# Performance work log

Measured on AMD Instinct MI355X. Metric: run time of the kernel, lower is better.

Reference implementation:

```python
import jax, jax.numpy as jnp
import numpy as np

N = 4096        # nodes
E = 131072      # edges (avg degree 32)
D = 128         # parser.d
H1, H2, H3 = 256, 128, 64   # parser.neurons_gnn
L = 2
THRESH = 0.6 ** L           # cosine-similarity cutoff used in attention()
SCALE = 0.05                # weight init scale


def setup_inputs() -> dict:
    key = jax.random.key(0)
    ks = jax.random.split(key, 14)
    X = jax.random.normal(ks[0], (N, D), dtype=jnp.float32)
    edge_index = jax.random.randint(ks[1], (2, E), 0, N, dtype=jnp.int64)
    W1 = jax.random.normal(ks[2], (D, H1), dtype=jnp.float32) * SCALE
    b1 = jnp.zeros((H1,), dtype=jnp.float32)
    a1w = jax.random.normal(ks[3], (2 * H1,), dtype=jnp.float32) * SCALE
    a1b = jnp.zeros((), dtype=jnp.float32)
    W2 = jax.random.normal(ks[4], (H1, H2), dtype=jnp.float32) * SCALE
    b2 = jnp.zeros((H2,), dtype=jnp.float32)
    a2w = jax.random.normal(ks[5], (2 * H2,), dtype=jnp.float32) * SCALE
    a2b = jnp.zeros((), dtype=jnp.float32)
    W3 = jax.random.normal(ks[6], (H2, H3), dtype=jnp.float32) * SCALE
    b3 = jnp.zeros((H3,), dtype=jnp.float32)
    return {"X": X, "edge_index": edge_index,
            "W1": W1, "b1": b1, "a1w": a1w, "a1b": a1b,
            "W2": W2, "b2": b2, "a2w": a2w, "a2b": a2b,
            "W3": W3, "b3": b3}


def _attention(h, src, dst, aw, ab):
    """Vectorized form of GNN.attention: edge-softmax neighbor aggregation
    plus dense cosine-thresholded all-pairs aggregation, averaged.
    attn_fc(cat(h_i, h_j)) = (h_i . aw_left) + (h_j . aw_right) + ab."""
    n, dh = h.shape
    al = h @ aw[:dh]            # [N] left half of attention projection
    ar = h @ aw[dh:]            # [N] right half
    # --- neighbor branch: a_ij = softmax-like normalized exp(leaky_relu(.)) over neighbors of i
    e = jnp.exp(jax.nn.leaky_relu(al[src] + ar[dst] + ab))   # [E]
    denom = jax.ops.segment_sum(e, src, num_segments=n)      # [N]
    a = e / denom[src]                                       # [E]
    h_a = h + jax.ops.segment_sum(a[:, None] * h[dst], src, num_segments=n)
    # --- dense branch: thresholded cosine similarity modulates attention score
    hn = h / jnp.linalg.norm(h, axis=1, keepdims=True)       # [N, dh]
    C = hn @ hn.T                                            # [N, N] cosine
    C = jnp.where(C <= THRESH, 0.0, C)
    S = al[:, None] + ar[None, :] + ab                       # [N, N] attn scores
    B = jnp.exp(C * jax.nn.leaky_relu(S))                    # [N, N]
    h1 = h + B @ h
    return 0.5 * (h_a + h1)


def reference(X, edge_index, W1, b1, a1w, a1b, W2, b2, a2w, a2b, W3, b3):
    src, dst = edge_index[0], edge_index[1]
    h = X @ W1 + b1
    h = _attention(h, src, dst, a1w, a1b)
    h = jax.nn.relu(h)
    h = h @ W2 + b2
    h = _attention(h, src, dst, a2w, a2b)
    h = jax.nn.relu(h)
    h = h @ W3 + b3
    # F.normalize(h, p=2, dim=1)
    h = h / jnp.maximum(jnp.linalg.norm(h, axis=1, keepdims=True), 1e-12)
    return h
```

## Files before the change

### kernel.cpp

```cpp
#include <hip/hip_runtime.h>
#include <math.h>
#include <type_traits>

#define NN 4096
#define NE 131072

typedef short short8 __attribute__((ext_vector_type(8)));
typedef float f32x4 __attribute__((ext_vector_type(4)));
typedef float f32x2 __attribute__((ext_vector_type(2)));
typedef unsigned short u16;

__device__ __forceinline__ float lrelu_f(float x) { return x > 0.0f ? x : 0.01f * x; }

__device__ __forceinline__ u16 f2bf(float x) {
  unsigned int u = __float_as_uint(x);
  unsigned int r = (u + 0x7FFF + ((u >> 16) & 1)) >> 16;
  return (u16)r;
}
__device__ __forceinline__ float bf2f(u16 b) { return __uint_as_float(((unsigned int)b) << 16); }

__device__ __forceinline__ void gload_lds16(const u16* g, u16* l) {
  __builtin_amdgcn_global_load_lds((const __attribute__((address_space(1))) void*)g,
                                   (__attribute__((address_space(3))) void*)l, 16, 0, 0);
}

__global__ __launch_bounds__(256) void wtrans_all_kernel(
    const float* __restrict__ W1, const float* __restrict__ W2, const float* __restrict__ W3,
    u16* __restrict__ w1h, u16* __restrict__ w1l,
    u16* __restrict__ w2h, u16* __restrict__ w2l,
    u16* __restrict__ w3h, u16* __restrict__ w3l) {
  __shared__ u16 th[32][33], tl[32][33];
  const float* W; u16 *oh, *ol; int K, P, bp, bk;
  int bx = blockIdx.x;
  if (bx < 32)      { W = W1; oh = w1h; ol = w1l; K = 128; P = 256; int b = bx;      bp = b & 7; bk = b >> 3; }
  else if (bx < 64) { W = W2; oh = w2h; ol = w2l; K = 256; P = 128; int b = bx - 32; bp = b & 3; bk = b >> 2; }
  else              { W = W3; oh = w3h; ol = w3l; K = 128; P = 64;  int b = bx - 64; bp = b & 1; bk = b >> 1; }
  int t = threadIdx.x, tx = t & 31, ty8 = t >> 5;
  #pragma unroll
  for (int r = 0; r < 4; ++r) {
    int k = bk * 32 + ty8 + r * 8;
    int p = bp * 32 + tx;
    float x = W[(size_t)k * P + p];
    u16 hi = f2bf(x);
    th[ty8 + r * 8][tx] = hi;
    tl[ty8 + r * 8][tx] = f2bf(x - bf2f(hi));
  }
  __syncthreads();
  #pragma unroll
  for (int r = 0; r < 4; ++r) {
    int p = bp * 32 + ty8 + r * 8;
    int k = bk * 32 + tx;
    oh[(size_t)p * K + k] = th[tx][ty8 + r * 8];
    ol[(size_t)p * K + k] = tl[tx][ty8 + r * 8];
  }
}

template<int K, int P, bool RELU, bool NORM>
__global__ __launch_bounds__(256) void mgemm_kernel(
    const float* __restrict__ A,
    const u16* __restrict__ WThi, const u16* __restrict__ WTlo,
    const float* __restrict__ bias, float* __restrict__ O) {
  constexpr int KC = K / 32;
  __shared__ float ldsn[4][16];
  int w = threadIdx.x >> 6, l = threadIdx.x & 63;
  int lr = l & 15, lk = l >> 4;
  int i0 = blockIdx.x * 16;
  int p0 = blockIdx.y * 64 + w * 16;
  const float* ar_ = A + (size_t)(i0 + lr) * K + lk * 8;
  const u16* brh = WThi + (size_t)(p0 + lr) * K + lk * 8;
  const u16* brl = WTlo + (size_t)(p0 + lr) * K + lk * 8;
  f32x4 ahh = {0.f, 0.f, 0.f, 0.f};
  f32x4 ahl = {0.f, 0.f, 0.f, 0.f};
  f32x4 alh = {0.f, 0.f, 0.f, 0.f};
  #pragma unroll
  for (int c = 0; c < KC; ++c) {
    f32x4 a0 = *(const f32x4*)(ar_ + 32 * c);
    f32x4 a1 = *(const f32x4*)(ar_ + 32 * c + 4);
    float av[8] = {a0[0], a0[1], a0[2], a0[3], a1[0], a1[1], a1[2], a1[3]};
    short8 Ah, Al;
    #pragma unroll
    for (int j = 0; j < 8; ++j) {
      float x = av[j];
      if (RELU) x = fmaxf(x, 0.0f);
      u16 hi = f2bf(x);
      Ah[j] = (short)hi;
      Al[j] = (short)f2bf(x - bf2f(hi));
    }
    short8 Bh = *(const short8*)(brh + 32 * c);
    short8 Bl = *(const short8*)(brl + 32 * c);
    ahh = __builtin_amdgcn_mfma_f32_16x16x32_bf16(Ah, Bh, ahh, 0, 0, 0);
    ahl = __builtin_amdgcn_mfma_f32_16x16x32_bf16(Ah, Bl, ahl, 0, 0, 0);
    alh = __builtin_amdgcn_mfma_f32_16x16x32_bf16(Al, Bh, alh, 0, 0, 0);
  }
  int p = p0 + lr;
  float bv = bias[p];
  float ov[4];
  #pragma unroll
  for (int q = 0; q < 4; ++q) ov[q] = ahh[q] + ahl[q] + alh[q] + bv;

  if (NORM) {
    float sq[4];
    #pragma unroll
    for (int q = 0; q < 4; ++q) {
      float s = ov[q] * ov[q];
      #pragma unroll
      for (int m = 1; m < 16; m <<= 1) s += __shfl_xor(s, m);
      sq[q] = s;
    }
    if (lr == 0) {
      #pragma unroll
      for (int q = 0; q < 4; ++q) ldsn[w][4 * lk + q] = sq[q];
    }
    __syncthreads();
    #pragma unroll
    for (int q = 0; q < 4; ++q) {
      int row = 4 * lk + q;
      float n2 = ldsn[0][row] + ldsn[1][row] + ldsn[2][row] + ldsn[3][row];
      float nf = 1.0f / fmaxf(sqrtf(n2), 1e-12f);
      int i = i0 + row;
      O[(size_t)i * P + p] = ov[q] * nf;
    }
  } else {
    #pragma unroll
    for (int q = 0; q < 4; ++q) {
      int i = i0 + 4 * lk + q;
      O[(size_t)i * P + p] = ov[q];
    }
  }
}

template<int DH>
__global__ __launch_bounds__(256) void prep_kernel(const float* __restrict__ h,
    const float* __restrict__ aw, float* __restrict__ al, float* __restrict__ ar,
    float* __restrict__ inv, float* __restrict__ cs,
    u16* __restrict__ hhi, u16* __restrict__ hlo, u16* __restrict__ hT) {
  constexpr int CPT = DH / 16;
  __shared__ u16 tile[16][DH + 8];
  __shared__ float ldsp[4][DH];
  int t = threadIdx.x;
  int w = t >> 6, l = t & 63;
  int rw = l >> 4;
  int row = w * 4 + rw;
  int tcol = l & 15;
  int i = blockIdx.x * 16 + row;
  int c0 = tcol * CPT;

  float v[CPT];
  const float* hr = h + (size_t)i * DH + c0;
  #pragma unroll
  for (int k = 0; k < CPT; k += 4) {
    f32x4 x = *(const f32x4*)(hr + k);
    v[k] = x[0]; v[k + 1] = x[1]; v[k + 2] = x[2]; v[k + 3] = x[3];
  }
  float s2 = 0.f, sl = 0.f, sr = 0.f;
  #pragma unroll
  for (int k = 0; k < CPT; ++k) {
    s2 = fmaf(v[k], v[k], s2);
    sl = fmaf(v[k], aw[c0 + k], sl);
    sr = fmaf(v[k], aw[DH + c0 + k], sr);
  }
  #pragma unroll
  for (int m = 1; m < 16; m <<= 1) {
    s2 += __shfl_xor(s2, m);
    sl += __shfl_xor(sl, m);
    sr += __shfl_xor(sr, m);
  }
  if (tcol == 0) { al[i] = sl; ar[i] = sr; inv[i] = rsqrtf(s2); }

  short8 hs[CPT / 8], ls[CPT / 8];
  #pragma unroll
  for (int k = 0; k < CPT; ++k) {
    float x = v[k];
    u16 hi = f2bf(x);
    hs[k / 8][k & 7] = (short)hi;
    ls[k / 8][k & 7] = (short)f2bf(x - bf2f(hi));
  }
  #pragma unroll
  for (int b = 0; b < CPT / 8; ++b) {
    *(short8*)&hhi[(size_t)i * DH + c0 + b * 8] = hs[b];
    *(short8*)&hlo[(size_t)i * DH + c0 + b * 8] = ls[b];
    *(short8*)&tile[row][c0 + b * 8] = hs[b];
  }
  float colp[CPT];
  #pragma unroll
  for (int k = 0; k < CPT; ++k) {
    float s = v[k];
    s += __shfl_xor(s, 16);
    s += __shfl_xor(s, 32);
    colp[k] = s;
  }
  if (rw == 0) {
    #pragma unroll
    for (int k = 0; k < CPT; ++k) ldsp[w][c0 + k] = colp[k];
  }
  __syncthreads();
  if (t < DH) {
    float s = ldsp[0][t] + ldsp[1][t] + ldsp[2][t] + ldsp[3][t];
    atomicAdd(&cs[t], s);
    int i0 = blockIdx.x * 16;
    short8 o0, o1;
    #pragma unroll
    for (int r = 0; r < 8; ++r) o0[r] = (short)tile[r][t];
    #pragma unroll
    for (int r = 0; r < 8; ++r) o1[r] = (short)tile[8 + r][t];
    *(short8*)&hT[(size_t)t * NN + i0] = o0;
    *(short8*)&hT[(size_t)t * NN + i0 + 8] = o1;
  }
}

__global__ void hist_kernel(const int* __restrict__ src, int* __restrict__ counts) {
  int e = blockIdx.x * 256 + threadIdx.x;
  atomicAdd(&counts[src[e]], 1);
}

__global__ __launch_bounds__(1024) void scan_kernel(const int* __restrict__ counts,
    int* __restrict__ offsets, int* __restrict__ cursor) {
  __shared__ int part[1024];
  int t = threadIdx.x;
  int v[4]; int run = 0;
  #pragma unroll
  for (int j = 0; j < 4; ++j) { v[j] = counts[4 * t + j]; run += v[j]; }
  part[t] = run;
  __syncthreads();
  for (int off = 1; off < 1024; off <<= 1) {
    int y = (t >= off) ? part[t - off] : 0;
    __syncthreads();
    part[t] += y;
    __syncthreads();
  }
  int base = part[t] - run;
  #pragma unroll
  for (int j = 0; j < 4; ++j) { offsets[4 * t + j] = base; cursor[4 * t + j] = base; base += v[j]; }
  if (t == 1023) offsets[NN] = base;
}

__global__ void scatter_idx_kernel(const int* __restrict__ src, const int* __restrict__ dst,
    int* __restrict__ cursor, int* __restrict__ dstS) {
  int e = blockIdx.x * 256 + threadIdx.x;
  int s = src[e];
  int p = atomicAdd(&cursor[s], 1);
  dstS[p] = dst[e];
}

template<int DH>
__global__ __launch_bounds__(256) void gather_kernel(const float* __restrict__ h,
    const int* __restrict__ offsets, const int* __restrict__ dstS,
    const float* __restrict__ al, const float* __restrict__ ar,
    const float* __restrict__ ab, float* __restrict__ o) {
  constexpr int VW = DH / 64;
  using V = typename std::conditional<VW == 4, f32x4, f32x2>::type;
  int wid = threadIdx.x >> 6, lane = threadIdx.x & 63;
  int i = blockIdx.x * 4 + wid;
  int beg = offsets[i], end = offsets[i + 1];
  float base = al[i] + ab[0];
  V acc0{}, acc1{};
  float esum0 = 0.f, esum1 = 0.f;
  int k = beg;
  for (; k + 2 <= end; k += 2) {
    int d0 = dstS[k], d1 = dstS[k + 1];
    float e0 = expf(lrelu_f(base + ar[d0]));
    float e1 = expf(lrelu_f(base + ar[d1]));
    V v0 = *(const V*)&h[(size_t)d0 * DH + lane * VW];
    V v1 = *(const V*)&h[(size_t)d1 * DH + lane * VW];
    esum0 += e0; esum1 += e1;
    acc0 += e0 * v0;
    acc1 += e1 * v1;
  }
  if (k < end) {
    int d0 = dstS[k];
    float e0 = expf(lrelu_f(base + ar[d0]));
    V v0 = *(const V*)&h[(size_t)d0 * DH + lane * VW];
    esum0 += e0;
    acc0 += e0 * v0;
  }
  float esum = esum0 + esum1;
  float rd = (beg < end) ? 0.5f / esum : 0.0f;
  *(V*)&o[(size_t)i * DH + lane * VW] = (acc0 + acc1) * rd;
}

template<int DH>
__global__ __launch_bounds__(256) void qk_kernel(
    const u16* __restrict__ hhi, const u16* __restrict__ hlo,
    const float* __restrict__ al, const float* __restrict__ ar,
    const float* __restrict__ inv, const float* __restrict__ ab,
    u16* __restrict__ W, int* __restrict__ flags) {
  constexpr int KC = DH / 32;
  __shared__ u16 sA[2][2][128][32];
  __shared__ u16 sB[2][2][128][32];
  int i0 = blockIdx.x * 128;
  int j0 = blockIdx.y * 128;
  int w = threadIdx.x >> 6, l = threadIdx.x & 63;
  int wr = w >> 1, wc = w & 1;
  int lr = l & 15, lk = l >> 4;

  int rl = l >> 2;
  int sc = ((l & 3) ^ ((l >> 3) & 3)) * 8;
  const u16* gAh0 = hhi + (size_t)(i0 + 32 * w + rl) * DH + sc;
  const u16* gAl0 = hlo + (size_t)(i0 + 32 * w + rl) * DH + sc;
  const u16* gBh0 = hhi + (size_t)(j0 + 32 * w + rl) * DH + sc;
  const u16* gBl0 = hlo + (size_t)(j0 + 32 * w + rl) * DH + sc;

  f32x4 acc[4][4];
  #pragma unroll
  for (int q = 0; q < 4; ++q)
    #pragma unroll
    for (int s = 0; s < 4; ++s) acc[q][s] = (f32x4){0.f, 0.f, 0.f, 0.f};

#define QK_STAGE(buf, c) do { \
    gload_lds16(gAh0 + (c) * 32,           &sA[buf][0][32 * w][0]); \
    gload_lds16(gAh0 + 16 * DH + (c) * 32, &sA[buf][0][32 * w + 16][0]); \
    gload_lds16(gAl0 + (c) * 32,           &sA[buf][1][32 * w][0]); \
    gload_lds16(gAl0 + 16 * DH + (c) * 32, &sA[buf][1][32 * w + 16][0]); \
    gload_lds16(gBh0 + (c) * 32,           &sB[buf][0][32 * w][0]); \
    gload_lds16(gBh0 + 16 * DH + (c) * 32, &sB[buf][0][32 * w + 16][0]); \
    gload_lds16(gBl0 + (c) * 32,           &sB[buf][1][32 * w][0]); \
    gload_lds16(gBl0 + 16 * DH + (c) * 32, &sB[buf][1][32 * w + 16][0]); \
  } while (0)

  QK_STAGE(0, 0);
  __syncthreads();

  int cs = (lk ^ ((lr >> 1) & 3)) * 8;
  int cur = 0;
  for (int c = 0; c < KC; ++c) {
    if (c + 1 < KC) QK_STAGE(cur ^ 1, c + 1);
    short8 Ah[4], Al[4], Bh[4], Bl[4];
    #pragma unroll
    for (int q = 0; q < 4; ++q) {
      Ah[q] = *(const short8*)&sA[cur][0][64 * wr + 16 * q + lr][cs];
      Al[q] = *(const short8*)&sA[cur][1][64 * wr + 16 * q + lr][cs];
    }
    #pragma unroll
    for (int s = 0; s < 4; ++s) {
      Bh[s] = *(const short8*)&sB[cur][0][64 * wc + 16 * s + lr][cs];
      Bl[s] = *(const short8*)&sB[cur][1][64 * wc + 16 * s + lr][cs];
    }
    #pragma unroll
    for (int q = 0; q < 4; ++q)
      #pragma unroll
      for (int s = 0; s < 4; ++s) {
        acc[q][s] = __builtin_amdgcn_mfma_f32_16x16x32_bf16(Al[q], Bh[s], acc[q][s], 0, 0, 0);
        acc[q][s] = __builtin_amdgcn_mfma_f32_16x16x32_bf16(Ah[q], Bl[s], acc[q][s], 0, 0, 0);
        acc[q][s] = __builtin_amdgcn_mfma_f32_16x16x32_bf16(Ah[q], Bh[s], acc[q][s], 0, 0, 0);
      }
    __syncthreads();
    cur ^= 1;
  }
#undef QK_STAGE

  float abv = ab[0];
  int i_base = i0 + 64 * wr + 4 * lk;
  int j_base = j0 + 64 * wc + lr;
  float invj[4];
  #pragma unroll
  for (int s = 0; s < 4; ++s) invj[s] = inv[j_base + 16 * s];
  float invi16[16];
  #pragma unroll
  for (int q = 0; q < 4; ++q)
    #pragma unroll
    for (int qq = 0; qq < 4; ++qq) invi16[4 * q + qq] = inv[i_base + 16 * q + qq];

  int wany = 0;
  #pragma unroll
  for (int q = 0; q < 4; ++q)
    #pragma unroll
    for (int s = 0; s < 4; ++s)
      #pragma unroll
      for (int qq = 0; qq < 4; ++qq) {
        float C = acc[q][s][qq] * invi16[4 * q + qq] * invj[s];
        if (C > 0.36f) wany = 1;
      }
  int anyv = __any(wany) ? 1 : 0;
  if (l == 0)
    flags[((i0 >> 6) + wr) * 64 + (j0 >> 6) + wc] = anyv;

  if (anyv) {
    float arj[4];
    #pragma unroll
    for (int s = 0; s < 4; ++s) arj[s] = ar[j_base + 16 * s] + abv;
    #pragma unroll
    for (int q = 0; q < 4; ++q) {
      float ali_[4];
      #pragma unroll
      for (int qq = 0; qq < 4; ++qq) ali_[qq] = al[i_base + 16 * q + qq];
      #pragma unroll
      for (int s = 0; s < 4; ++s)
        #pragma unroll
        for (int qq = 0; qq < 4; ++qq) {
          float C = acc[q][s][qq] * invi16[4 * q + qq] * invj[s];
          float wv = 0.0f;
          if (C > 0.36f) wv = expm1f(C * lrelu_f(ali_[qq] + arj[s]));
          W[(size_t)(i_base + 16 * q + qq) * NN + j_base + 16 * s] = f2bf(wv);
        }
    }
  }
}

template<int DH>
__global__ __launch_bounds__(256) void pv_kernel(
    const u16* __restrict__ W, const u16* __restrict__ hT,
    const int* __restrict__ flags, const float* __restrict__ h,
    const float* __restrict__ cs, float* __restrict__ o) {
  __shared__ u16 sW[2][16][64];
  __shared__ u16 sT[2][4][16][64];
  __shared__ int list[64];
  __shared__ int nact_s;
  int ib = blockIdx.x;
  int w = threadIdx.x >> 6, l = threadIdx.x & 63;
  int lr = l & 15, lk = l >> 4;
  int i0 = ib * 16;
  int d0 = blockIdx.y * 64 + w * 16;
  const int* frow = flags + (i0 >> 6) * 64;
  if (threadIdx.x < 64) {
    int f = frow[threadIdx.x] != 0;
    unsigned long long m = __ballot(f);
    int pos = __popcll(m & ((1ULL << threadIdx.x) - 1ULL));
    if (f) list[pos] = threadIdx.x;
    if (threadIdx.x == 0) nact_s = __popcll(m);
  }
  __syncthreads();
  int nact = nact_s;

  int srow0 = l >> 3;
  int scol = ((l & 7) * 8) ^ ((srow0 & 7) << 3);
  const u16* gW0 = W + (size_t)(i0 + srow0) * NN + scol;
  const u16* gT0 = hT + (size_t)(d0 + srow0) * NN + scol;
  f32x4 acc0 = {0.f, 0.f, 0.f, 0.f};
  f32x4 acc1 = {0.f, 0.f, 0.f, 0.f};

  if (nact > 0) {
    {
      int j0 = list[0] * 64;
      if (w == 0) {
        gload_lds16(gW0 + j0, &sW[0][0][0]);
        gload_lds16(gW0 + 8 * NN + j0, &sW[0][8][0]);
      }
      gload_lds16(gT0 + j0, &sT[0][w][0][0]);
      gload_lds16(gT0 + 8 * NN + j0, &sT[0][w][8][0]);
    }
    __syncthreads();
    int cur = 0;
    for (int t = 0; t < nact; ++t) {
      if (t + 1 < nact) {
        int jn = list[t + 1] * 64;
        int nb = cur ^ 1;
        if (w == 0) {
          gload_lds16(gW0 + jn, &sW[nb][0][0]);
          gload_lds16(gW0 + 8 * NN + jn, &sW[nb][8][0]);
        }
        gload_lds16(gT0 + jn, &sT[nb][w][0][0]);
        gload_lds16(gT0 + 8 * NN + jn, &sT[nb][w][8][0]);
      }
      int sx = (lr & 7) << 3;
      short8 a0 = *(const short8*)&sW[cur][lr][(lk * 8) ^ sx];
      short8 a1 = *(const short8*)&sW[cur][lr][(32 + lk * 8) ^ sx];
      short8 b0 = *(const short8*)&sT[cur][w][lr][(lk * 8) ^ sx];
      short8 b1 = *(const short8*)&sT[cur][w][lr][(32 + lk * 8) ^ sx];
      acc0 = __builtin_amdgcn_mfma_f32_16x16x32_bf16(a0, b0, acc0, 0, 0, 0);
      acc1 = __builtin_amdgcn_mfma_f32_16x16x32_bf16(a1, b1, acc1, 0, 0, 0);
      __syncthreads();
      cur ^= 1;
    }
  }

  int d = d0 + lr;
  #pragma unroll
  for (int q = 0; q < 4; ++q) {
    int i = i0 + 4 * lk + q;
    size_t idx = (size_t)i * DH + d;
    o[idx] = o[idx] + h[idx] + 0.5f * cs[d] + 0.5f * (acc0[q] + acc1[q]);
  }
}

struct Scratch {
  float *al, *ar, *inv, *cs1, *cs2;
  int *counts, *offsets, *cursor, *dstS, *flags;
  u16 *hhi, *hlo, *hT, *W;
  u16 *w1h, *w1l, *w2h, *w2l, *w3h, *w3l;
};

template<int DH>
static void run_attention(const float* h, const float* aw, const float* ab, float* o,
                          float* cs, const Scratch& S, hipStream_t stream) {
  prep_kernel<DH><<<NN / 16, 256, 0, stream>>>(h, aw, S.al, S.ar, S.inv, cs,
                                               S.hhi, S.hlo, S.hT);
  gather_kernel<DH><<<NN / 4, 256, 0, stream>>>(h, S.offsets, S.dstS, S.al, S.ar, ab, o);
  qk_kernel<DH><<<dim3(NN / 128, NN / 128), 256, 0, stream>>>(
      S.hhi, S.hlo, S.al, S.ar, S.inv, ab, S.W, S.flags);
  pv_kernel<DH><<<dim3(NN / 16, DH / 64), 256, 0, stream>>>(
      S.W, S.hT, S.flags, h, cs, o);
}

extern "C" void kernel_launch(void* const* d_in, const int* in_sizes, int n_in,
                              void* d_out, int out_size, void* d_ws, size_t ws_size,
                              hipStream_t stream) {
  const float* X   = (const float*)d_in[0];
  const int*   ei  = (const int*)d_in[1];
  const float* W1  = (const float*)d_in[2];
  const float* b1  = (const float*)d_in[3];
  const float* a1w = (const float*)d_in[4];
  const float* a1b = (const float*)d_in[5];
  const float* W2  = (const float*)d_in[6];
  const float* b2  = (const float*)d_in[7];
  const float* a2w = (const float*)d_in[8];
  const float* a2b = (const float*)d_in[9];
  const float* W3  = (const float*)d_in[10];
  const float* b3  = (const float*)d_in[11];
  float* out = (float*)d_out;

  const int* src = ei;
  const int* dst = ei + NE;

  char* p = (char*)d_ws;
  auto alloc = [&](size_t bytes) { char* r = p; p += (bytes + 255) & ~(size_t)255; return r; };
  float* h1 = (float*)alloc((size_t)NN * 256 * 4);
  float* o1 = (float*)alloc((size_t)NN * 256 * 4);
  float* h2 = (float*)alloc((size_t)NN * 128 * 4);
  float* o2 = (float*)alloc((size_t)NN * 128 * 4);
  Scratch S;
  S.counts = (int*)alloc(NN * 4);
  S.cs1    = (float*)alloc(256 * 4);
  S.cs2    = (float*)alloc(128 * 4);
  S.hhi = (u16*)alloc((size_t)NN * 256 * 2);
  S.hlo = (u16*)alloc((size_t)NN * 256 * 2);
  S.hT  = (u16*)alloc((size_t)NN * 256 * 2);
  S.W   = (u16*)alloc((size_t)NN * NN * 2);
  S.w1h = (u16*)alloc((size_t)256 * 128 * 2);
  S.w1l = (u16*)alloc((size_t)256 * 128 * 2);
  S.w2h = (u16*)alloc((size_t)128 * 256 * 2);
  S.w2l = (u16*)alloc((size_t)128 * 256 * 2);
  S.w3h = (u16*)alloc((size_t)64 * 128 * 2);
  S.w3l = (u16*)alloc((size_t)64 * 128 * 2);
  S.flags = (int*)alloc(4096 * 4);
  S.al    = (float*)alloc(NN * 4);
  S.ar    = (float*)alloc(NN * 4);
  S.inv   = (float*)alloc(NN * 4);
  S.offsets = (int*)alloc((NN + 1) * 4);
  S.cursor  = (int*)alloc(NN * 4);
  S.dstS    = (int*)alloc((size_t)NE * 4);

  hipMemsetAsync(S.counts, 0, NN * 4 + 256 * 4 + 128 * 4, stream);
  hist_kernel<<<NE / 256, 256, 0, stream>>>(src, S.counts);
  scan_kernel<<<1, 1024, 0, stream>>>(S.counts, S.offsets, S.cursor);
  scatter_idx_kernel<<<NE / 256, 256, 0, stream>>>(src, dst, S.cursor, S.dstS);
  wtrans_all_kernel<<<72, 256, 0, stream>>>(W1, W2, W3,
      S.w1h, S.w1l, S.w2h, S.w2l, S.w3h, S.w3l);

  mgemm_kernel<128, 256, false, false><<<dim3(NN / 16, 256 / 64), 256, 0, stream>>>(
      X, S.w1h, S.w1l, b1, h1);
  run_attention<256>(h1, a1w, a1b, o1, S.cs1, S, stream);

  mgemm_kernel<256, 128, true, false><<<dim3(NN / 16, 128 / 64), 256, 0, stream>>>(
      o1, S.w2h, S.w2l, b2, h2);
  run_attention<128>(h2, a2w, a2b, o2, S.cs2, S, stream);

  mgemm_kernel<128, 64, true, true><<<dim3(NN / 16, 64 / 64), 256, 0, stream>>>(
      o2, S.w3h, S.w3l, b3, out);
}
```

Measured before the change: 253.9 us.

## Load low bf16 halves directly from global in qk kernel and swizzle block order

The QK cosine-similarity kernel now stages only the high bf16 halves of both operands through LDS. The low halves are read straight from global memory into registers each K step, which halves LDS footprint and staging traffic and may raise occupancy. It also remaps block indices in groups of 8 to improve L2 locality across the 2D grid. The trade-off is higher global and L2 read traffic and more load latency exposed in the MFMA loop, since those direct loads are not double-buffered.

```diff
diff --git a/kernel.cpp b/kernel.cpp
--- a/kernel.cpp
+++ b/kernel.cpp
@@ -285,10 +285,14 @@
     const float* __restrict__ inv, const float* __restrict__ ab,
     u16* __restrict__ W, int* __restrict__ flags) {
   constexpr int KC = DH / 32;
-  __shared__ u16 sA[2][2][128][32];
-  __shared__ u16 sB[2][2][128][32];
-  int i0 = blockIdx.x * 128;
-  int j0 = blockIdx.y * 128;
+  __shared__ u16 sA[2][128][32];
+  __shared__ u16 sB[2][128][32];
+  int lin = blockIdx.y * gridDim.x + blockIdx.x;
+  int cpx = (gridDim.x * gridDim.y) >> 3;
+  int swz = (lin & 7) * cpx + (lin >> 3);
+  int bi = swz / gridDim.x, bj = swz % gridDim.x;
+  int i0 = bi * 128;
+  int j0 = bj * 128;
   int w = threadIdx.x >> 6, l = threadIdx.x & 63;
   int wr = w >> 1, wc = w & 1;
   int lr = l & 15, lk = l >> 4;
@@ -296,9 +300,9 @@
   int rl = l >> 2;
   int sc = ((l & 3) ^ ((l >> 3) & 3)) * 8;
   const u16* gAh0 = hhi + (size_t)(i0 + 32 * w + rl) * DH + sc;
-  const u16* gAl0 = hlo + (size_t)(i0 + 32 * w + rl) * DH + sc;
   const u16* gBh0 = hhi + (size_t)(j0 + 32 * w + rl) * DH + sc;
-  const u16* gBl0 = hlo + (size_t)(j0 + 32 * w + rl) * DH + sc;
+  const u16* pAl = hlo + (size_t)(i0 + 64 * wr + lr) * DH + lk * 8;
+  const u16* pBl = hlo + (size_t)(j0 + 64 * wc + lr) * DH + lk * 8;
 
   f32x4 acc[4][4];
   #pragma unroll
@@ -307,14 +311,10 @@
     for (int s = 0; s < 4; ++s) acc[q][s] = (f32x4){0.f, 0.f, 0.f, 0.f};
 
 #define QK_STAGE(buf, c) do { \
-    gload_lds16(gAh0 + (c) * 32,           &sA[buf][0][32 * w][0]); \
-    gload_lds16(gAh0 + 16 * DH + (c) * 32, &sA[buf][0][32 * w + 16][0]); \
-    gload_lds16(gAl0 + (c) * 32,           &sA[buf][1][32 * w][0]); \
-    gload_lds16(gAl0 + 16 * DH + (c) * 32, &sA[buf][1][32 * w + 16][0]); \
-    gload_lds16(gBh0 + (c) * 32,           &sB[buf][0][32 * w][0]); \
-    gload_lds16(gBh0 + 16 * DH + (c) * 32, &sB[buf][0][32 * w + 16][0]); \
-    gload_lds16(gBl0 + (c) * 32,           &sB[buf][1][32 * w][0]); \
-    gload_lds16(gBl0 + 16 * DH + (c) * 32, &sB[buf][1][32 * w + 16][0]); \
+    gload_lds16(gAh0 + (c) * 32,           &sA[buf][32 * w][0]); \
+    gload_lds16(gAh0 + 16 * DH + (c) * 32, &sA[buf][32 * w + 16][0]); \
+    gload_lds16(gBh0 + (c) * 32,           &sB[buf][32 * w][0]); \
+    gload_lds16(gBh0 + 16 * DH + (c) * 32, &sB[buf][32 * w + 16][0]); \
   } while (0)
 
   QK_STAGE(0, 0);
@@ -324,17 +324,18 @@
   int cur = 0;
   for (int c = 0; c < KC; ++c) {
     if (c + 1 < KC) QK_STAGE(cur ^ 1, c + 1);
-    short8 Ah[4], Al[4], Bh[4], Bl[4];
-    #pragma unroll
-    for (int q = 0; q < 4; ++q) {
-      Ah[q] = *(const short8*)&sA[cur][0][64 * wr + 16 * q + lr][cs];
-      Al[q] = *(const short8*)&sA[cur][1][64 * wr + 16 * q + lr][cs];
-    }
-    #pragma unroll
-    for (int s = 0; s < 4; ++s) {
-      Bh[s] = *(const short8*)&sB[cur][0][64 * wc + 16 * s + lr][cs];
-      Bl[s] = *(const short8*)&sB[cur][1][64 * wc + 16 * s + lr][cs];
-    }
+    short8 Al[4], Bl[4];
+    #pragma unroll
+    for (int q = 0; q < 4; ++q) Al[q] = *(const short8*)(pAl + (size_t)(16 * q) * DH + c * 32);
+    #pragma unroll
+    for (int s = 0; s < 4; ++s) Bl[s] = *(const short8*)(pBl + (size_t)(16 * s) * DH + c * 32);
+    short8 Ah[4], Bh[4];
+    #pragma unroll
+    for (int q = 0; q < 4; ++q)
+      Ah[q] = *(const short8*)&sA[cur][64 * wr + 16 * q + lr][cs];
+    #pragma unroll
+    for (int s = 0; s < 4; ++s)
+      Bh[s] = *(const short8*)&sB[cur][64 * wc + 16 * s + lr][cs];
     #pragma unroll
     for (int q = 0; q < 4; ++q)
       #pragma unroll
```

Result: slower. 272.9 us (+7.5%).
